# Optimization experiments

Measured on AMD Instinct MI355X. Metric: run time of the kernel, lower is better.

The kernel has to match this reference:

```python
import jax, jax.numpy as jnp
import numpy as np

B, C, T, F = 4, 2, 4224, 256
L = 256          # sequence_len (block size over time)
STRIDE = 128
H = 8            # num_heads
RF = L // 2      # receptive_field default


def setup_inputs() -> dict:
    key = jax.random.key(0)
    k0, k1, k2, k3, k4 = jax.random.split(key, 5)
    s = 0.05
    return {
        "x": jax.random.normal(k0, (B, C, T, F), dtype=jnp.float32),
        "w_in": jax.random.normal(k1, (3 * F, F), dtype=jnp.float32) * s,
        "b_in": jax.random.normal(k2, (3 * F,), dtype=jnp.float32) * s,
        "w_out": jax.random.normal(k3, (F, F), dtype=jnp.float32) * s,
        "b_out": jax.random.normal(k4, (F,), dtype=jnp.float32) * s,
    }


def reference(x, w_in, b_in, w_out, b_out):
    b, c, t, f = x.shape
    nb = (t - L) // STRIDE + 1              # num_blocks
    dh = f // H                              # head dim

    # --- UnfoldSpectrogram: (B,C,T,F) -> (B,C,nb,L,F) ---
    idx = jnp.arange(nb)[:, None] * STRIDE + jnp.arange(L)[None, :]  # (nb, L)
    blocks = x[:, :, idx, :]                 # (B,C,nb,L,F)

    # --- MultiheadAttention over flattened batch of blocks ---
    xb = blocks.reshape(b * c * nb, L, f)    # (N,L,F)
    qkv = xb @ w_in.T + b_in                 # (N,L,3F)
    q, k, v = jnp.split(qkv, 3, axis=-1)
    q = q.reshape(-1, L, H, dh)
    k = k.reshape(-1, L, H, dh)
    v = v.reshape(-1, L, H, dh)

    scale = 1.0 / np.sqrt(dh).astype(np.float32)
    scores = jnp.einsum("nihd,njhd->nhij", q, k) * scale  # (N,H,L,L)

    # Faithful to the original: the Longformer mask is a FLOAT 0/1 tensor that
    # torch's MultiheadAttention ADDS to the scores (band gets +1.0).
    di = jnp.arange(L)[:, None] - jnp.arange(L)[None, :]
    band = ((di >= 0) & (di < RF)).astype(scores.dtype)   # (L,L)
    scores = scores + band

    attn = jax.nn.softmax(scores, axis=-1)
    o = jnp.einsum("nhij,njhd->nihd", attn, v).reshape(-1, L, f)
    o = o @ w_out.T + b_out                  # (N,L,F)

    # --- FoldSpectrogram: overlap-add then normalize by overlap count ---
    ob = o.reshape(b, c, nb, L, f)
    y = jnp.zeros((b, c, t, f), dtype=o.dtype).at[:, :, idx, :].add(ob)
    cnt = jnp.zeros((t,), dtype=o.dtype).at[idx.reshape(-1)].add(1.0)
    return y / cnt[None, None, :, None]
```

## Files before the change

### kernel.cpp

```cpp
#include <hip/hip_runtime.h>

typedef unsigned short u16;
typedef unsigned int u32;
typedef __attribute__((ext_vector_type(8))) short bf16x8;
typedef __attribute__((ext_vector_type(4))) float f32x4;
typedef __attribute__((ext_vector_type(4))) u32 u32x4;
typedef __attribute__((ext_vector_type(2))) u32 u32x2;

__device__ __forceinline__ u16 f2bf(float f) {
  u32 u = __builtin_bit_cast(u32, f);
  return (u16)((u + 0x7FFFu + ((u >> 16) & 1u)) >> 16);
}
__device__ __forceinline__ float bf2f(u16 b) {
  return __builtin_bit_cast(float, (u32)b << 16);
}

__device__ __forceinline__ float fexp2(float x) {
#if __has_builtin(__builtin_amdgcn_exp2f)
  return __builtin_amdgcn_exp2f(x);
#else
  return __expf(x * 0.6931471805599453f);
#endif
}

__device__ __forceinline__ void lds_async16(const void* g, void* l) {
  auto gp = reinterpret_cast<const __attribute__((address_space(1))) u32*>(
      reinterpret_cast<uintptr_t>(g));
  auto lp = reinterpret_cast<__attribute__((address_space(3))) u32*>(
      reinterpret_cast<uintptr_t>(l));
  __builtin_amdgcn_global_load_lds(gp, lp, 16, 0, 0);
}

__global__ void cvt_kernel(const float* __restrict__ in, u16* __restrict__ out, int n4) {
  int i = blockIdx.x * 256 + threadIdx.x;
  if (i < n4) {
    f32x4 v = *(const f32x4*)(in + (size_t)i * 4);
    u32x2 o;
    o[0] = (u32)f2bf(v[0]) | ((u32)f2bf(v[1]) << 16);
    o[1] = (u32)f2bf(v[2]) | ((u32)f2bf(v[3]) << 16);
    *(u32x2*)(out + (size_t)i * 4) = o;
  }
}

__global__ void cvt2_kernel(const float* __restrict__ a, const float* __restrict__ b,
                            u16* __restrict__ oa, u16* __restrict__ ob, int na4, int nb4) {
  int i = blockIdx.x * 256 + threadIdx.x;
  const float* src;
  u16* dst;
  int idx;
  if (i < na4) {
    src = a; dst = oa; idx = i;
  } else {
    idx = i - na4;
    if (idx >= nb4) return;
    src = b; dst = ob;
  }
  f32x4 v = *(const f32x4*)(src + (size_t)idx * 4);
  u32x2 o;
  o[0] = (u32)f2bf(v[0]) | ((u32)f2bf(v[1]) << 16);
  o[1] = (u32)f2bf(v[2]) | ((u32)f2bf(v[3]) << 16);
  *(u32x2*)(dst + (size_t)idx * 4) = o;
}

template <bool OUT_BF16>
__global__ __launch_bounds__(256) void gemm_bt_kernel(
    const u16* __restrict__ A, const u16* __restrict__ B,
    const float* __restrict__ bias, void* __restrict__ C,
    int M, int N, int K) {
  __shared__ u16 sA[128 * 32];
  __shared__ u16 sB[128 * 32];
  const int tid = threadIdx.x;
  const int m0 = blockIdx.x * 128;
  const int n0 = blockIdx.y * 128;
  const int w = tid >> 6;
  const int lane = tid & 63;
  const int wr = (w >> 1) * 64;
  const int wc = (w & 1) * 64;
  const int lm = lane & 15;
  const int lk = (lane >> 4) * 8;

  f32x4 acc[4][4] = {};

  const int srow = tid >> 2;
  const int ssub = (tid & 3) * 8;
  const u16* Ag = A + (size_t)(m0 + srow) * K + ssub;
  const u16* Bg = B + (size_t)(n0 + srow) * K + ssub;
  const size_t rstep = (size_t)64 * K;

  for (int k0 = 0; k0 < K; k0 += 32) {
    __syncthreads();
    lds_async16(Ag + k0, &sA[tid * 8]);
    lds_async16(Ag + rstep + k0, &sA[2048 + tid * 8]);
    lds_async16(Bg + k0, &sB[tid * 8]);
    lds_async16(Bg + rstep + k0, &sB[2048 + tid * 8]);
    __syncthreads();
    bf16x8 af[4], bfr[4];
#pragma unroll
    for (int i = 0; i < 4; ++i)
      af[i] = *(const bf16x8*)&sA[(wr + i * 16 + lm) * 32 + lk];
#pragma unroll
    for (int j = 0; j < 4; ++j)
      bfr[j] = *(const bf16x8*)&sB[(wc + j * 16 + lm) * 32 + lk];
#pragma unroll
    for (int i = 0; i < 4; ++i)
#pragma unroll
      for (int j = 0; j < 4; ++j)
        acc[i][j] = __builtin_amdgcn_mfma_f32_16x16x32_bf16(af[i], bfr[j], acc[i][j], 0, 0, 0);
  }

  const int r0 = (lane >> 4) * 4;
#pragma unroll
  for (int j = 0; j < 4; ++j) {
    const int n = n0 + wc + j * 16 + lm;
    const float bv = bias[n];
#pragma unroll
    for (int i = 0; i < 4; ++i) {
#pragma unroll
      for (int r = 0; r < 4; ++r) {
        const int m = m0 + wr + i * 16 + r0 + r;
        float v = acc[i][j][r] + bv;
        if (OUT_BF16)
          ((u16*)C)[(size_t)m * N + n] = f2bf(v);
        else
          ((float*)C)[(size_t)m * N + n] = v;
      }
    }
  }
}

__global__ __launch_bounds__(256, 2) void attn_kernel(const u16* __restrict__ qkv,
                                                      u16* __restrict__ o_ws) {
  __shared__ u16 sVt[32 * 264];
  __shared__ u16 sP[4 * 32 * 40];

  const int bid = blockIdx.x;
  const int n = bid >> 3;
  const int h = bid & 7;
  const int rowbase = (n >> 5) * 4224 + (n & 31) * 128;
  const int tid = threadIdx.x;
  const int w = tid >> 6;
  const int lane = tid & 63;
  const int lm = lane & 15;
  const int lg = lane >> 4;

#pragma unroll
  for (int it = 0; it < 4; ++it) {
    int c = it * 256 + tid;
    int row = c >> 2;
    int sub = (c & 3) * 8;
    const u16* gv = qkv + (size_t)(rowbase + row) * 768 + 512 + h * 32 + sub;
    u32x4 vv = *(const u32x4*)gv;
#pragma unroll
    for (int q = 0; q < 4; ++q) {
      sVt[(sub + 2 * q) * 264 + row] = (u16)(vv[q] & 0xFFFFu);
      sVt[(sub + 2 * q + 1) * 264 + row] = (u16)(vv[q] >> 16);
    }
  }

  bf16x8 qf[4];
#pragma unroll
  for (int rt = 0; rt < 4; ++rt) {
    int row = rowbase + w * 64 + rt * 16 + lm;
    qf[rt] = *(const bf16x8*)(qkv + (size_t)row * 768 + h * 32 + lg * 8);
  }

  __syncthreads();

  f32x4 oacc[4][2] = {};
  float lsum[4] = {0.f, 0.f, 0.f, 0.f};
  u16* myP = sP + w * (32 * 40);
  const float C1 = 0.25500035370494726f;
  const float C2 = 1.4426950408889634f;
  const int jq = lg * 4;
  const u16* kbase = qkv + (size_t)(rowbase + lm) * 768 + 256 + h * 32 + lg * 8;
  const int D0w = w * 64;

#pragma unroll 1
  for (int ch = 0; ch < 8; ++ch) {
    bf16x8 kf[2], vf[2];
#pragma unroll
    for (int ct = 0; ct < 2; ++ct)
      kf[ct] = *(const bf16x8*)(kbase + (size_t)(ch * 32 + ct * 16) * 768);
#pragma unroll
    for (int ctd = 0; ctd < 2; ++ctd)
      vf[ctd] = *(const bf16x8*)&sVt[(ctd * 16 + lm) * 264 + ch * 32 + lg * 8];

#pragma unroll
    for (int hf = 0; hf < 2; ++hf) {
#pragma unroll
      for (int ct = 0; ct < 2; ++ct) {
#pragma unroll
        for (int rl = 0; rl < 2; ++rl) {
          const int rt = hf * 2 + rl;
          f32x4 s = __builtin_amdgcn_mfma_f32_16x16x32_bf16(kf[ct], qf[rt], f32x4{0.f, 0.f, 0.f, 0.f}, 0, 0, 0);
          const int D0 = D0w + rt * 16 - (ch * 32 + ct * 16);
          float p0, p1, p2, p3;
          if (D0 >= 16 && D0 <= 112) {
            p0 = fexp2(__builtin_fmaf(s[0], C1, C2));
            p1 = fexp2(__builtin_fmaf(s[1], C1, C2));
            p2 = fexp2(__builtin_fmaf(s[2], C1, C2));
            p3 = fexp2(__builtin_fmaf(s[3], C1, C2));
          } else if (D0 == 0) {
            p0 = fexp2(__builtin_fmaf(s[0], C1, (lm >= jq + 0) ? C2 : 0.0f));
            p1 = fexp2(__builtin_fmaf(s[1], C1, (lm >= jq + 1) ? C2 : 0.0f));
            p2 = fexp2(__builtin_fmaf(s[2], C1, (lm >= jq + 2) ? C2 : 0.0f));
            p3 = fexp2(__builtin_fmaf(s[3], C1, (lm >= jq + 3) ? C2 : 0.0f));
          } else if (D0 == 128) {
            p0 = fexp2(__builtin_fmaf(s[0], C1, (lm < jq + 0) ? C2 : 0.0f));
            p1 = fexp2(__builtin_fmaf(s[1], C1, (lm < jq + 1) ? C2 : 0.0f));
            p2 = fexp2(__builtin_fmaf(s[2], C1, (lm < jq + 2) ? C2 : 0.0f));
            p3 = fexp2(__builtin_fmaf(s[3], C1, (lm < jq + 3) ? C2 : 0.0f));
          } else {
            p0 = fexp2(s[0] * C1);
            p1 = fexp2(s[1] * C1);
            p2 = fexp2(s[2] * C1);
            p3 = fexp2(s[3] * C1);
          }
          lsum[rt] += (p0 + p1) + (p2 + p3);
          u32 u0 = __builtin_bit_cast(u32, p0) + 0x8000u;
          u32 u1 = __builtin_bit_cast(u32, p1) + 0x8000u;
          u32 u2 = __builtin_bit_cast(u32, p2) + 0x8000u;
          u32 u3 = __builtin_bit_cast(u32, p3) + 0x8000u;
          u32x2 pk;
          pk[0] = __builtin_amdgcn_perm(u1, u0, 0x07060302u);
          pk[1] = __builtin_amdgcn_perm(u3, u2, 0x07060302u);
          *(u32x2*)&myP[(rl * 16 + lm) * 40 + ct * 16 + jq] = pk;
        }
      }
      bf16x8 pf[2];
#pragma unroll
      for (int rl = 0; rl < 2; ++rl)
        pf[rl] = *(const bf16x8*)&myP[(rl * 16 + lm) * 40 + lg * 8];
      __asm__ __volatile__("" ::: "memory");
#pragma unroll
      for (int rl = 0; rl < 2; ++rl)
#pragma unroll
        for (int ctd = 0; ctd < 2; ++ctd)
          oacc[hf * 2 + rl][ctd] =
              __builtin_amdgcn_mfma_f32_16x16x32_bf16(pf[rl], vf[ctd], oacc[hf * 2 + rl][ctd], 0, 0, 0);
    }
  }

  float linv[4];
#pragma unroll
  for (int rt = 0; rt < 4; ++rt) {
    float v = lsum[rt];
    v += __shfl_xor(v, 16);
    v += __shfl_xor(v, 32);
    linv[rt] = 1.0f / v;
  }

#pragma unroll
  for (int rt = 0; rt < 4; ++rt) {
#pragma unroll
    for (int r = 0; r < 4; ++r) {
      float inv = __shfl(linv[rt], jq + r);
      int i_g = w * 64 + rt * 16 + jq + r;
#pragma unroll
      for (int ctd = 0; ctd < 2; ++ctd) {
        float v = oacc[rt][ctd][r] * inv;
        u32 u = __builtin_bit_cast(u32, v) + 0x8000u;
        o_ws[((size_t)(n * 256 + i_g)) * 256 + h * 32 + ctd * 16 + lm] = (u16)(u >> 16);
      }
    }
  }
}

__global__ void combine_kernel(const u16* __restrict__ o_ws, u16* __restrict__ oc) {
  int gid = blockIdx.x * 256 + threadIdx.x;
  int m = gid >> 5;
  int f0 = (gid & 31) << 3;
  int bc = m / 4224;
  int t = m - bc * 4224;
  int i0 = t >> 7;
  float a[8] = {0.f, 0.f, 0.f, 0.f, 0.f, 0.f, 0.f, 0.f};
  if (i0 <= 31) {
    const u16* p = o_ws + ((size_t)((bc * 32 + i0) * 256 + (t - (i0 << 7)))) * 256 + f0;
    u32x4 v = *(const u32x4*)p;
#pragma unroll
    for (int q = 0; q < 4; ++q) {
      a[2 * q] += bf2f((u16)(v[q] & 0xFFFFu));
      a[2 * q + 1] += bf2f((u16)(v[q] >> 16));
    }
  }
  if (i0 >= 1) {
    int i1 = i0 - 1;
    const u16* p = o_ws + ((size_t)((bc * 32 + i1) * 256 + (t - (i1 << 7)))) * 256 + f0;
    u32x4 v = *(const u32x4*)p;
#pragma unroll
    for (int q = 0; q < 4; ++q) {
      a[2 * q] += bf2f((u16)(v[q] & 0xFFFFu));
      a[2 * q + 1] += bf2f((u16)(v[q] >> 16));
    }
  }
  float sc = (i0 >= 1 && i0 <= 31) ? 0.5f : 1.0f;
  u32x2 o;
  o[0] = (u32)f2bf(a[0] * sc) | ((u32)f2bf(a[1] * sc) << 16);
  o[1] = (u32)f2bf(a[2] * sc) | ((u32)f2bf(a[3] * sc) << 16);
  u32x2 o2;
  o2[0] = (u32)f2bf(a[4] * sc) | ((u32)f2bf(a[5] * sc) << 16);
  o2[1] = (u32)f2bf(a[6] * sc) | ((u32)f2bf(a[7] * sc) << 16);
  u16* dst = oc + (size_t)m * 256 + f0;
  *(u32x2*)dst = o;
  *(u32x2*)(dst + 4) = o2;
}

extern "C" void kernel_launch(void* const* d_in, const int* in_sizes, int n_in,
                              void* d_out, int out_size, void* d_ws, size_t ws_size,
                              hipStream_t stream) {
  const float* x = (const float*)d_in[0];
  const float* w_in = (const float*)d_in[1];
  const float* b_in = (const float*)d_in[2];
  const float* w_out = (const float*)d_in[3];
  const float* b_out = (const float*)d_in[4];
  float* y = (float*)d_out;
  char* ws = (char*)d_ws;

  u16* qkv = (u16*)(ws);
  u16* xbf = (u16*)(ws + 51904512);
  u16* ows = (u16*)(ws + 69206016);
  u16* winb = (u16*)(ws + 102760448);
  u16* woutb = (u16*)(ws + 103153664);

  cvt_kernel<<<8448, 256, 0, stream>>>(x, xbf, 2162688);
  cvt2_kernel<<<256, 256, 0, stream>>>(w_in, w_out, winb, woutb, 49152, 16384);

  gemm_bt_kernel<true><<<dim3(264, 6), 256, 0, stream>>>(xbf, winb, b_in, qkv, 33792, 768, 256);

  attn_kernel<<<2048, 256, 0, stream>>>(qkv, ows);

  combine_kernel<<<4224, 256, 0, stream>>>(ows, xbf);

  gemm_bt_kernel<false><<<dim3(264, 2), 256, 0, stream>>>(xbf, woutb, b_out, y, 33792, 256, 256);
}
```

Baseline: 186.7 us.

## Prefetch K fragments, swizzle V^T LDS, compute softmax row sums via MFMA

Adds XOR swizzling to the transposed V tile in LDS to cut bank conflicts, and prefetches the next chunk's K fragments from global memory one iteration ahead to hide load latency. The softmax denominator is now accumulated by an MFMA of the bf16 P tile against a ones vector rather than by scalar adds and cross-lane shuffles, so the sum uses the same rounded P values as the PV product. Float-to-bf16 packing switches to the hardware v_cvt_pk_bf16_f32 instruction, and s_setprio is raised around the PV MFMAs. The ones-MFMA adds matrix-core work per chunk in exchange for fewer VALU and shuffle instructions.

```diff
diff --git a/kernel.cpp b/kernel.cpp
--- a/kernel.cpp
+++ b/kernel.cpp
@@ -148,12 +148,13 @@
     int c = it * 256 + tid;
     int row = c >> 2;
     int sub = (c & 3) * 8;
+    int rsw = row ^ ((sub >> 3) << 4);
     const u16* gv = qkv + (size_t)(rowbase + row) * 768 + 512 + h * 32 + sub;
     u32x4 vv = *(const u32x4*)gv;
 #pragma unroll
     for (int q = 0; q < 4; ++q) {
-      sVt[(sub + 2 * q) * 264 + row] = (u16)(vv[q] & 0xFFFFu);
-      sVt[(sub + 2 * q + 1) * 264 + row] = (u16)(vv[q] >> 16);
+      sVt[(sub + 2 * q) * 264 + rsw] = (u16)(vv[q] & 0xFFFFu);
+      sVt[(sub + 2 * q + 1) * 264 + rsw] = (u16)(vv[q] >> 16);
     }
   }
 
@@ -164,26 +165,37 @@
     qf[rt] = *(const bf16x8*)(qkv + (size_t)row * 768 + h * 32 + lg * 8);
   }
 
+  const u16* kbase = qkv + (size_t)(rowbase + lm) * 768 + 256 + h * 32 + lg * 8;
+
+  bf16x8 kfc[2];
+#pragma unroll
+  for (int ct = 0; ct < 2; ++ct)
+    kfc[ct] = *(const bf16x8*)(kbase + (size_t)(ct * 16) * 768);
+
   __syncthreads();
 
   f32x4 oacc[4][2] = {};
-  float lsum[4] = {0.f, 0.f, 0.f, 0.f};
+  f32x4 lacc[4] = {};
   u16* myP = sP + w * (32 * 40);
   const float C1 = 0.25500035370494726f;
   const float C2 = 1.4426950408889634f;
   const int jq = lg * 4;
-  const u16* kbase = qkv + (size_t)(rowbase + lm) * 768 + 256 + h * 32 + lg * 8;
   const int D0w = w * 64;
+  const bf16x8 onesb = {(short)0x3F80, (short)0x3F80, (short)0x3F80, (short)0x3F80,
+                        (short)0x3F80, (short)0x3F80, (short)0x3F80, (short)0x3F80};
 
 #pragma unroll 1
   for (int ch = 0; ch < 8; ++ch) {
-    bf16x8 kf[2], vf[2];
+    const int chn = (ch < 7) ? ch + 1 : 7;
+    bf16x8 kfn[2], vf[2];
 #pragma unroll
     for (int ct = 0; ct < 2; ++ct)
-      kf[ct] = *(const bf16x8*)(kbase + (size_t)(ch * 32 + ct * 16) * 768);
-#pragma unroll
-    for (int ctd = 0; ctd < 2; ++ctd)
-      vf[ctd] = *(const bf16x8*)&sVt[(ctd * 16 + lm) * 264 + ch * 32 + lg * 8];
+      kfn[ct] = *(const bf16x8*)(kbase + (size_t)(chn * 32 + ct * 16) * 768);
+#pragma unroll
+    for (int ctd = 0; ctd < 2; ++ctd) {
+      int d = ctd * 16 + lm;
+      vf[ctd] = *(const bf16x8*)&sVt[d * 264 + ((ch * 32 + lg * 8) ^ ((d >> 3) << 4))];
+    }
 
 #pragma unroll
     for (int hf = 0; hf < 2; ++hf) {
@@ -192,7 +204,7 @@
 #pragma unroll
         for (int rl = 0; rl < 2; ++rl) {
           const int rt = hf * 2 + rl;
-          f32x4 s = __builtin_amdgcn_mfma_f32_16x16x32_bf16(kf[ct], qf[rt], f32x4{0.f, 0.f, 0.f, 0.f}, 0, 0, 0);
+          f32x4 s = __builtin_amdgcn_mfma_f32_16x16x32_bf16(kfc[ct], qf[rt], f32x4{0.f, 0.f, 0.f, 0.f}, 0, 0, 0);
           const int D0 = D0w + rt * 16 - (ch * 32 + ct * 16);
           float p0, p1, p2, p3;
           if (D0 >= 16 && D0 <= 112) {
@@ -216,14 +228,12 @@
             p2 = fexp2(s[2] * C1);
             p3 = fexp2(s[3] * C1);
           }
-          lsum[rt] += (p0 + p1) + (p2 + p3);
-          u32 u0 = __builtin_bit_cast(u32, p0) + 0x8000u;
-          u32 u1 = __builtin_bit_cast(u32, p1) + 0x8000u;
-          u32 u2 = __builtin_bit_cast(u32, p2) + 0x8000u;
-          u32 u3 = __builtin_bit_cast(u32, p3) + 0x8000u;
+          u32 a0, a1;
+          asm("v_cvt_pk_bf16_f32 %0, %1, %2" : "=v"(a0) : "v"(p0), "v"(p1));
+          asm("v_cvt_pk_bf16_f32 %0, %1, %2" : "=v"(a1) : "v"(p2), "v"(p3));
           u32x2 pk;
-          pk[0] = __builtin_amdgcn_perm(u1, u0, 0x07060302u);
-          pk[1] = __builtin_amdgcn_perm(u3, u2, 0x07060302u);
+          pk[0] = a0;
+          pk[1] = a1;
           *(u32x2*)&myP[(rl * 16 + lm) * 40 + ct * 16 + jq] = pk;
         }
       }
@@ -232,29 +242,27 @@
       for (int rl = 0; rl < 2; ++rl)
         pf[rl] = *(const bf16x8*)&myP[(rl * 16 + lm) * 40 + lg * 8];
       __asm__ __volatile__("" ::: "memory");
-#pragma unroll
-      for (int rl = 0; rl < 2; ++rl)
+      __builtin_amdgcn_s_setprio(1);
+#pragma unroll
+      for (int rl = 0; rl < 2; ++rl) {
+        lacc[hf * 2 + rl] =
+            __builtin_amdgcn_mfma_f32_16x16x32_bf16(pf[rl], onesb, lacc[hf * 2 + rl], 0, 0, 0);
 #pragma unroll
         for (int ctd = 0; ctd < 2; ++ctd)
           oacc[hf * 2 + rl][ctd] =
               __builtin_amdgcn_mfma_f32_16x16x32_bf16(pf[rl], vf[ctd], oacc[hf * 2 + rl][ctd], 0, 0, 0);
-    }
-  }
-
-  float linv[4];
+      }
+      __builtin_amdgcn_s_setprio(0);
+    }
+    kfc[0] = kfn[0];
+    kfc[1] = kfn[1];
+  }
+
 #pragma unroll
   for (int rt = 0; rt < 4; ++rt) {
-    float v = lsum[rt];
-    v += __shfl_xor(v, 16);
-    v += __shfl_xor(v, 32);
-    linv[rt] = 1.0f / v;
-  }
-
-#pragma unroll
-  for (int rt = 0; rt < 4; ++rt) {
 #pragma unroll
     for (int r = 0; r < 4; ++r) {
-      float inv = __shfl(linv[rt], jq + r);
+      float inv = 1.0f / lacc[rt][r];
       int i_g = w * 64 + rt * 16 + jq + r;
 #pragma unroll
       for (int ctd = 0; ctd < 2; ++ctd) {
```

Result: no change. 184.1 us (-1.4%).
